# Performance work log

Measured on AMD Instinct MI355X. Metric: run time of the kernel, lower is better.

## Reference

```python
import jax, jax.numpy as jnp
import numpy as np

N_NODES = 100000
N_EDGES = 1000000
NEG_SLOPE = 0.2


def gat_conv(x, src, dst, W, al, ar, b, res, activation):
    """DGL-style GATConv. res is None (no residual), 'id' (identity residual), or a [in,H*D] matrix."""
    H, D = al.shape
    n = x.shape[0]
    feat = (x @ W).reshape(n, H, D)                      # [N,H,D]
    el = jnp.einsum('nhd,hd->nh', feat, al)              # [N,H]
    er = jnp.einsum('nhd,hd->nh', feat, ar)              # [N,H]
    e = jax.nn.leaky_relu(el[src] + er[dst], NEG_SLOPE)  # [E,H]
    # edge softmax over incoming edges of each dst node
    m = jax.lax.stop_gradient(jax.ops.segment_max(e, dst, num_segments=n))
    ex = jnp.exp(e - m[dst])
    s = jax.ops.segment_sum(ex, dst, num_segments=n)
    alpha = ex / s[dst]                                  # [E,H]
    out = jax.ops.segment_sum(feat[src] * alpha[:, :, None], dst, num_segments=n)  # [N,H,D]
    if res == 'id':
        out = out + x.reshape(n, H, D)
    elif res is not None:
        out = out + (x @ res).reshape(n, H, D)
    out = out + b.reshape(1, H, D)
    if activation is not None:
        out = activation(out)
    return out


def setup_inputs() -> dict:
    key = jax.random.key(0)
    ks = jax.random.split(key, 20)
    F_IN, HID = 128, 32
    H1, H2, H3 = 4, 4, 1
    C = 40
    sc = 0.1
    inp = {
        'x':   jax.random.normal(ks[0], (N_NODES, F_IN), dtype=jnp.float32),
        'src': jax.random.randint(ks[1], (N_EDGES,), 0, N_NODES, dtype=jnp.int32),
        'dst': jax.random.randint(ks[2], (N_EDGES,), 0, N_NODES, dtype=jnp.int32),
        # layer 1: in=128 -> H1*HID=128, no residual, elu
        'W1':  sc * jax.random.normal(ks[3], (F_IN, H1 * HID), dtype=jnp.float32),
        'al1': sc * jax.random.normal(ks[4], (H1, HID), dtype=jnp.float32),
        'ar1': sc * jax.random.normal(ks[5], (H1, HID), dtype=jnp.float32),
        'b1':  jnp.zeros((H1 * HID,), dtype=jnp.float32),
        # layer 2: in=128 -> H2*HID=128, identity residual, elu
        'W2':  sc * jax.random.normal(ks[6], (H1 * HID, H2 * HID), dtype=jnp.float32),
        'al2': sc * jax.random.normal(ks[7], (H2, HID), dtype=jnp.float32),
        'ar2': sc * jax.random.normal(ks[8], (H2, HID), dtype=jnp.float32),
        'b2':  jnp.zeros((H2 * HID,), dtype=jnp.float32),
        # layer 3 (output): in=128 -> H3*HID=32, projected residual, no activation
        'W3':  sc * jax.random.normal(ks[9], (H2 * HID, H3 * HID), dtype=jnp.float32),
        'al3': sc * jax.random.normal(ks[10], (H3, HID), dtype=jnp.float32),
        'ar3': sc * jax.random.normal(ks[11], (H3, HID), dtype=jnp.float32),
        'b3':  jnp.zeros((H3 * HID,), dtype=jnp.float32),
        'res3': sc * jax.random.normal(ks[12], (H2 * HID, H3 * HID), dtype=jnp.float32),
        # final classifier
        'Wfc': sc * jax.random.normal(ks[13], (HID, C), dtype=jnp.float32),
        'bfc': jnp.zeros((C,), dtype=jnp.float32),
    }
    return inp


def reference(x, src, dst, W1, al1, ar1, b1, W2, al2, ar2, b2, W3, al3, ar3, b3, res3, Wfc, bfc):
    n = x.shape[0]
    h = gat_conv(x, src, dst, W1, al1, ar1, b1, None, jax.nn.elu).reshape(n, -1)   # [N, 128]
    h = gat_conv(h, src, dst, W2, al2, ar2, b2, 'id', jax.nn.elu).reshape(n, -1)   # [N, 128]
    h = gat_conv(h, src, dst, W3, al3, ar3, b3, res3, None).mean(axis=1)           # [N, 32]
    return h @ Wfc + bfc                                                           # [N, 40]
```

## Files before the change

kernel.cpp:

```cpp
#include <hip/hip_runtime.h>
#include <cstdint>
#include <cstddef>

#define NN 100000
#define NE 1000000
#define GEMM_BLOCKS 1563
#define TICKET_BLOCKS 3907
#define NB_SCAN 391
#define LOG2E 1.4426950408896340736f

typedef unsigned int uint;
typedef unsigned short ushort;
typedef __attribute__((ext_vector_type(8))) short bfrag;
typedef __attribute__((ext_vector_type(4))) float f32x4;

__device__ __forceinline__ ushort f2bf(float f){
  uint u = __float_as_uint(f);
  u += 0x7fffu + ((u >> 16) & 1u);
  return (ushort)(u >> 16);
}
__device__ __forceinline__ float bflo(uint p){ return __uint_as_float(p << 16); }
__device__ __forceinline__ float bfhi(uint p){ return __uint_as_float(p & 0xffff0000u); }


__device__ __forceinline__ void bfrag_body(const float* __restrict__ B1, const float* __restrict__ B2,
                                           int n1, int n2, int NT, ushort* __restrict__ out, int i){
  if (i >= NT*4*64) return;
  int l = i & 63, ks = (i>>6)&3, nt = i>>8;
  int col = nt*16 + (l&15);
  int k0  = ks*32 + (l>>4)*8;
  const float* B; int stride, c;
  if (col < n1){ B = B1; stride = n1; c = col; }
  else         { B = B2; stride = n2; c = col - n1; }
  ushort v[8];
  #pragma unroll
  for (int j=0;j<8;j++) v[j] = f2bf(B[(size_t)(k0+j)*stride + c]);
  uint4 pk;
  pk.x = (uint)v[0] | ((uint)v[1]<<16);
  pk.y = (uint)v[2] | ((uint)v[3]<<16);
  pk.z = (uint)v[4] | ((uint)v[5]<<16);
  pk.w = (uint)v[6] | ((uint)v[7]<<16);
  *(uint4*)(out + (size_t)i*8) = pk;
}

__global__ __launch_bounds__(256) void k_packs(const float* __restrict__ W1, const float* __restrict__ W2,
                                               const float* __restrict__ W3, const float* __restrict__ res3,
                                               ushort* __restrict__ Bf1, ushort* __restrict__ Bf2,
                                               ushort* __restrict__ Bf3){
  int r = blockIdx.x, t = threadIdx.x;
  if (r < 8)       bfrag_body(W1, nullptr, 128, 0, 8, Bf1, r*256 + t);
  else if (r < 16) bfrag_body(W2, nullptr, 128, 0, 8, Bf2, (r-8)*256 + t);
  else             bfrag_body(W3, res3,    32, 32, 4, Bf3, (r-16)*256 + t);
}


__global__ __launch_bounds__(256, 4)
void k_gemm1_ticket(const float* __restrict__ x, const ushort* __restrict__ Bf1,
                    ushort* __restrict__ featb,
                    const float* __restrict__ al, const float* __restrict__ ar,
                    float* __restrict__ el, float* __restrict__ er,
                    const int* __restrict__ dst, int* __restrict__ cnt4, int* __restrict__ tick){
  int bid = blockIdx.x, t = threadIdx.x;
  if (bid >= GEMM_BLOCKS){
    int e = (bid - GEMM_BLOCKS)*256 + t;
    if (e < NE) tick[e] = atomicAdd(&cnt4[(uint)dst[e]*4u + (e & 3)], 1);
    return;
  }

  int l = t & 63, w = t >> 6;
  int rw = bid*64 + w*16;
  int c = l & 15, g = l >> 4;

  f32x4 acc[8];
  #pragma unroll
  for (int nt=0;nt<8;nt++) acc[nt] = (f32x4){0.f,0.f,0.f,0.f};

  int rowA = rw + c; if (rowA >= NN) rowA = NN-1;
  const float* Ap = x + (size_t)rowA*128 + g*8;
  const bfrag* Bp = (const bfrag*)Bf1;

  #pragma unroll
  for (int ks=0; ks<4; ++ks){
    float4 f0 = *(const float4*)(Ap + ks*32);
    float4 f1 = *(const float4*)(Ap + ks*32 + 4);
    bfrag a;
    a[0]=(short)f2bf(f0.x); a[1]=(short)f2bf(f0.y); a[2]=(short)f2bf(f0.z); a[3]=(short)f2bf(f0.w);
    a[4]=(short)f2bf(f1.x); a[5]=(short)f2bf(f1.y); a[6]=(short)f2bf(f1.z); a[7]=(short)f2bf(f1.w);
    #pragma unroll
    for (int nt=0; nt<8; ++nt){
      bfrag b = Bp[(nt*4+ks)*64 + l];
      acc[nt] = __builtin_amdgcn_mfma_f32_16x16x32_bf16(a, b, acc[nt], 0, 0, 0);
    }
  }

  float alv[4][2], arv[4][2];
  #pragma unroll
  for (int h=0;h<4;h++){
    alv[h][0]=al[h*32+c]*LOG2E;    arv[h][0]=ar[h*32+c]*LOG2E;
    alv[h][1]=al[h*32+16+c]*LOG2E; arv[h][1]=ar[h*32+16+c]*LOG2E;
  }

  #pragma unroll
  for (int reg=0; reg<4; ++reg){
    int row = rw + g*4 + reg;
    bool ok = row < NN;
    #pragma unroll
    for (int h=0;h<4;h++){
      float pl = acc[2*h][reg]*alv[h][0] + acc[2*h+1][reg]*alv[h][1];
      float pr = acc[2*h][reg]*arv[h][0] + acc[2*h+1][reg]*arv[h][1];
      #pragma unroll
      for (int off=1; off<16; off<<=1){ pl += __shfl_xor(pl,off); pr += __shfl_xor(pr,off); }
      if (ok && c==0){ el[(size_t)row*4 + h] = pl; er[(size_t)row*4 + h] = pr; }
    }
    if (ok){
      #pragma unroll
      for (int nt=0; nt<8; ++nt)
        featb[(size_t)row*128 + nt*16 + c] = f2bf(acc[nt][reg]);
    }
  }
}


__global__ __launch_bounds__(256) void k_scan_local(const int* __restrict__ cnt4, int* __restrict__ shoff,
                                                    int* __restrict__ rowptr, int* __restrict__ bsum){
  __shared__ int sm[256];
  int t = threadIdx.x;
  int i = blockIdx.x*256 + t;
  int v = 0;
  if (i < NN){
    int4 cc = ((const int4*)cnt4)[i];
    v = cc.x + cc.y + cc.z + cc.w;
    int4 so;
    so.x = 0; so.y = cc.x; so.z = cc.x + cc.y; so.w = cc.x + cc.y + cc.z;
    ((int4*)shoff)[i] = so;
  }
  sm[t] = v;
  __syncthreads();
  for (int off=1; off<256; off<<=1){
    int u = (t>=off) ? sm[t-off] : 0;
    __syncthreads();
    sm[t] += u;
    __syncthreads();
  }
  if (i < NN) rowptr[i] = sm[t] - v;
  if (t == 255) bsum[blockIdx.x] = sm[255];
}

__global__ __launch_bounds__(512) void k_scan_finish(int* __restrict__ rowptr, const int* __restrict__ bsum){
  __shared__ int sm[512];
  __shared__ int ex[512];
  int t = threadIdx.x;
  int v = (t < NB_SCAN) ? bsum[t] : 0;
  sm[t] = v;
  __syncthreads();
  for (int off=1; off<512; off<<=1){
    int u = (t>=off) ? sm[t-off] : 0;
    __syncthreads();
    sm[t] += u;
    __syncthreads();
  }
  ex[t] = sm[t] - v;
  __syncthreads();
  int i = blockIdx.x*512 + t;
  if (i < NN) rowptr[i] += ex[i>>8];
  else if (i == NN) rowptr[NN] = NE;
}


__global__ __launch_bounds__(256) void k_place_dhist(const int* __restrict__ src, const int* __restrict__ dst,
                                                     const int* __restrict__ rowptr, const int* __restrict__ shoff,
                                                     const int* __restrict__ tick, int* __restrict__ csr,
                                                     int* __restrict__ dbin){
  __shared__ int lh[256];
  int bid = blockIdx.x, t = threadIdx.x;
  if (bid < TICKET_BLOCKS){
    int e = bid*256 + t;
    if (e < NE){
      int d = dst[e];
      csr[rowptr[d] + shoff[(uint)d*4u + (e & 3)] + tick[e]] = src[e];
    }
  } else {
    lh[t] = 0;
    __syncthreads();
    int n = (bid - TICKET_BLOCKS)*256 + t;
    if (n < NN){
      int deg = rowptr[n+1] - rowptr[n];
      atomicAdd(&lh[deg > 255 ? 255 : deg], 1);
    }
    __syncthreads();
    if (lh[t] > 0) atomicAdd(&dbin[t], lh[t]);
  }
}

__global__ __launch_bounds__(256) void k_dscan(int* __restrict__ dbin){
  __shared__ int sm[256];
  int t = threadIdx.x;
  int v = dbin[t];
  sm[t] = v;
  __syncthreads();
  for (int off=1; off<256; off<<=1){
    int u = (t>=off) ? sm[t-off] : 0;
    __syncthreads();
    sm[t] += u;
    __syncthreads();
  }
  dbin[t] = sm[t] - v;
}

__global__ __launch_bounds__(256) void k_dscat(const int* __restrict__ rowptr, int* __restrict__ dbin,
                                               int* __restrict__ perm){
  __shared__ int lh[256];
  __shared__ int lbase[256];
  int t = threadIdx.x;
  lh[t] = 0;
  __syncthreads();
  int n = blockIdx.x*256 + t;
  int bin = -1, lticket = 0;
  if (n < NN){
    int deg = rowptr[n+1] - rowptr[n];
    bin = deg > 255 ? 255 : deg;
    lticket = atomicAdd(&lh[bin], 1);
  }
  __syncthreads();
  if (lh[t] > 0) lbase[t] = atomicAdd(&dbin[t], lh[t]);
  __syncthreads();
  if (n < NN) perm[lbase[bin] + lticket] = n;
}


template<int NT, int NTF, int H>
__device__ __forceinline__ void gemm_body(int bid, const ushort* __restrict__ Ab, const ushort* __restrict__ Bf,
                                          ushort* __restrict__ featb, float* __restrict__ Cres,
                                          const float* __restrict__ al, const float* __restrict__ ar,
                                          float* __restrict__ el, float* __restrict__ er, int M){
  __shared__ ushort Bs[NT*2048];
  int t = threadIdx.x;
  #pragma unroll
  for (int i=0; i<NT; ++i)
    ((uint4*)Bs)[i*256 + t] = ((const uint4*)Bf)[i*256 + t];
  __syncthreads();

  int l = t & 63, w = t >> 6;
  int rw = bid*64 + w*16;
  int c = l & 15, g = l >> 4;

  f32x4 acc[NT];
  #pragma unroll
  for (int nt=0;nt<NT;nt++) acc[nt] = (f32x4){0.f,0.f,0.f,0.f};

  int rowA = rw + c; if (rowA >= M) rowA = M-1;
  const ushort* Ap = Ab + (size_t)rowA*128 + g*8;
  const bfrag* Bp = (const bfrag*)Bs;

  #pragma unroll
  for (int ks=0; ks<4; ++ks){
    bfrag a = *(const bfrag*)(Ap + ks*32);
    #pragma unroll
    for (int nt=0; nt<NT; ++nt){
      bfrag b = Bp[(nt*4+ks)*64 + l];
      acc[nt] = __builtin_amdgcn_mfma_f32_16x16x32_bf16(a, b, acc[nt], 0, 0, 0);
    }
  }

  float alv[H][2], arv[H][2];
  #pragma unroll
  for (int h=0;h<H;h++){
    alv[h][0]=al[h*32+c]*LOG2E;    arv[h][0]=ar[h*32+c]*LOG2E;
    alv[h][1]=al[h*32+16+c]*LOG2E; arv[h][1]=ar[h*32+16+c]*LOG2E;
  }

  #pragma unroll
  for (int reg=0; reg<4; ++reg){
    int row = rw + g*4 + reg;
    bool ok = row < M;
    #pragma unroll
    for (int h=0;h<H;h++){
      float pl = acc[2*h][reg]*alv[h][0] + acc[2*h+1][reg]*alv[h][1];
      float pr = acc[2*h][reg]*arv[h][0] + acc[2*h+1][reg]*arv[h][1];
      #pragma unroll
      for (int off=1; off<16; off<<=1){ pl += __shfl_xor(pl,off); pr += __shfl_xor(pr,off); }
      if (ok && c==0){ el[(size_t)row*H + h] = pl; er[(size_t)row*H + h] = pr; }
    }
    if (ok){
      #pragma unroll
      for (int nt=0; nt<NTF; ++nt)
        featb[(size_t)row*(NTF*16) + nt*16 + c] = f2bf(acc[nt][reg]);
      #pragma unroll
      for (int nt=NTF; nt<NT; ++nt)
        Cres[(size_t)row*((NT-NTF)*16) + (nt-NTF)*16 + c] = acc[nt][reg];
    }
  }
}

template<int NT, int NTF, int H>
__global__ __launch_bounds__(256) void k_gemm_mfma(const ushort* __restrict__ Ab, const ushort* __restrict__ Bf,
                                                   ushort* __restrict__ featb, float* __restrict__ Cres,
                                                   const float* __restrict__ al, const float* __restrict__ ar,
                                                   float* __restrict__ el, float* __restrict__ er, int M){
  gemm_body<NT,NTF,H>(blockIdx.x, Ab, Bf, featb, Cres, al, ar, el, er, M);
}


template<int RK>
__global__ __launch_bounds__(256) void k_agg4(const int* __restrict__ rowptr, const int* __restrict__ csr,
                                              const int* __restrict__ perm,
                                              const ushort* __restrict__ feat,
                                              const float* __restrict__ el, const float* __restrict__ er,
                                              const void* __restrict__ res, const float* __restrict__ bias,
                                              ushort* __restrict__ out, int act){
  int t = threadIdx.x;
  int l15 = t & 15;
  int node = perm[blockIdx.x*16 + (t>>4)];

  int beg = rowptr[node], deg = rowptr[node+1] - beg;
  int hm = l15 >> 2;
  float erh = er[(size_t)node*4 + hm];
  const int* cp = csr + beg;
  uint fo = (uint)l15*8u;

  float ssum = 0.f;
  float a0=0.f,a1=0.f,a2=0.f,a3=0.f,a4=0.f,a5=0.f,a6=0.f,a7=0.f;

  int ei = 0;
  for (; ei+4 <= deg; ei += 4){
    int s0 = cp[ei], s1 = cp[ei+1], s2 = cp[ei+2], s3 = cp[ei+3];
    uint4 p0 = *(const uint4*)(feat + ((uint)s0*128u + fo));
    uint4 p1 = *(const uint4*)(feat + ((uint)s1*128u + fo));
    uint4 p2 = *(const uint4*)(feat + ((uint)s2*128u + fo));
    uint4 p3 = *(const uint4*)(feat + ((uint)s3*128u + fo));
    float v0 = el[(uint)s0*4u + hm] + erh; v0 = fmaxf(v0, 0.2f*v0);
    float v1 = el[(uint)s1*4u + hm] + erh; v1 = fmaxf(v1, 0.2f*v1);
    float v2 = el[(uint)s2*4u + hm] + erh; v2 = fmaxf(v2, 0.2f*v2);
    float v3 = el[(uint)s3*4u + hm] + erh; v3 = fmaxf(v3, 0.2f*v3);
    float w0 = __builtin_amdgcn_exp2f(v0);
    float w1 = __builtin_amdgcn_exp2f(v1);
    float w2 = __builtin_amdgcn_exp2f(v2);
    float w3 = __builtin_amdgcn_exp2f(v3);
    ssum += (w0 + w1) + (w2 + w3);
    a0 += w0*bflo(p0.x) + w1*bflo(p1.x) + w2*bflo(p2.x) + w3*bflo(p3.x);
    a1 += w0*bfhi(p0.x) + w1*bfhi(p1.x) + w2*bfhi(p2.x) + w3*bfhi(p3.x);
    a2 += w0*bflo(p0.y) + w1*bflo(p1.y) + w2*bflo(p2.y) + w3*bflo(p3.y);
    a3 += w0*bfhi(p0.y) + w1*bfhi(p1.y) + w2*bfhi(p2.y) + w3*bfhi(p3.y);
    a4 += w0*bflo(p0.z) + w1*bflo(p1.z) + w2*bflo(p2.z) + w3*bflo(p3.z);
    a5 += w0*bfhi(p0.z) + w1*bfhi(p1.z) + w2*bfhi(p2.z) + w3*bfhi(p3.z);
    a6 += w0*bflo(p0.w) + w1*bflo(p1.w) + w2*bflo(p2.w) + w3*bflo(p3.w);
    a7 += w0*bfhi(p0.w) + w1*bfhi(p1.w) + w2*bfhi(p2.w) + w3*bfhi(p3.w);
  }
  for (; ei < deg; ++ei){
    int s0 = cp[ei];
    uint4 p0 = *(const uint4*)(feat + ((uint)s0*128u + fo));
    float v0 = el[(uint)s0*4u + hm] + erh; v0 = fmaxf(v0, 0.2f*v0);
    float w0 = __builtin_amdgcn_exp2f(v0);
    ssum += w0;
    a0 += w0*bflo(p0.x); a1 += w0*bfhi(p0.x);
    a2 += w0*bflo(p0.y); a3 += w0*bfhi(p0.y);
    a4 += w0*bflo(p0.z); a5 += w0*bfhi(p0.z);
    a6 += w0*bflo(p0.w); a7 += w0*bfhi(p0.w);
  }

  float inv = (deg > 0) ? 1.f/ssum : 0.f;
  float o0=a0*inv, o1=a1*inv, o2=a2*inv, o3=a3*inv;
  float o4=a4*inv, o5=a5*inv, o6=a6*inv, o7=a7*inv;
  if (RK == 1){
    uint4 rv = *(const uint4*)((const ushort*)res + (size_t)node*128 + fo);
    o0 += bflo(rv.x); o1 += bfhi(rv.x); o2 += bflo(rv.y); o3 += bfhi(rv.y);
    o4 += bflo(rv.z); o5 += bfhi(rv.z); o6 += bflo(rv.w); o7 += bfhi(rv.w);
  }
  float4 bv0 = *(const float4*)(bias + l15*8);
  float4 bv1 = *(const float4*)(bias + l15*8 + 4);
  o0 += bv0.x; o1 += bv0.y; o2 += bv0.z; o3 += bv0.w;
  o4 += bv1.x; o5 += bv1.y; o6 += bv1.z; o7 += bv1.w;
  if (act){
    o0 = (o0>0.f)?o0:__expf(o0)-1.f;
    o1 = (o1>0.f)?o1:__expf(o1)-1.f;
    o2 = (o2>0.f)?o2:__expf(o2)-1.f;
    o3 = (o3>0.f)?o3:__expf(o3)-1.f;
    o4 = (o4>0.f)?o4:__expf(o4)-1.f;
    o5 = (o5>0.f)?o5:__expf(o5)-1.f;
    o6 = (o6>0.f)?o6:__expf(o6)-1.f;
    o7 = (o7>0.f)?o7:__expf(o7)-1.f;
  }
  uint4 pk;
  pk.x = (uint)f2bf(o0) | ((uint)f2bf(o1)<<16);
  pk.y = (uint)f2bf(o2) | ((uint)f2bf(o3)<<16);
  pk.z = (uint)f2bf(o4) | ((uint)f2bf(o5)<<16);
  pk.w = (uint)f2bf(o6) | ((uint)f2bf(o7)<<16);
  *(uint4*)(out + (size_t)node*128 + fo) = pk;
}


__global__ __launch_bounds__(256) void k_agg1(const int* __restrict__ rowptr, const int* __restrict__ csr,
                                              const int* __restrict__ perm,
                                              const ushort* __restrict__ feat,
                                              const float* __restrict__ el, const float* __restrict__ er,
                                              const float* __restrict__ res, const float* __restrict__ bias,
                                              float* __restrict__ h3){
  int t = threadIdx.x;
  int l7 = t & 7;
  int node = perm[blockIdx.x*32 + (t>>3)];

  int beg = rowptr[node], deg = rowptr[node+1] - beg;
  float er0 = er[node];
  const int* cp = csr + beg;
  uint fo = (uint)l7*4u;

  float ssum = 0.f, a0=0.f, a1=0.f, a2=0.f, a3=0.f;
  int ei = 0;
  for (; ei+2 <= deg; ei += 2){
    int s0 = cp[ei], s1 = cp[ei+1];
    uint2 p0 = *(const uint2*)(feat + ((uint)s0*32u + fo));
    uint2 p1 = *(const uint2*)(feat + ((uint)s1*32u + fo));
    float v0 = el[s0] + er0; v0 = fmaxf(v0, 0.2f*v0);
    float v1 = el[s1] + er0; v1 = fmaxf(v1, 0.2f*v1);
    float w0 = __builtin_amdgcn_exp2f(v0);
    float w1 = __builtin_amdgcn_exp2f(v1);
    ssum += w0 + w1;
    a0 += w0*bflo(p0.x) + w1*bflo(p1.x);
    a1 += w0*bfhi(p0.x) + w1*bfhi(p1.x);
    a2 += w0*bflo(p0.y) + w1*bflo(p1.y);
    a3 += w0*bfhi(p0.y) + w1*bfhi(p1.y);
  }
  if (ei < deg){
    int s0 = cp[ei];
    uint2 p0 = *(const uint2*)(feat + ((uint)s0*32u + fo));
    float v0 = el[s0] + er0; v0 = fmaxf(v0, 0.2f*v0);
    float w0 = __builtin_amdgcn_exp2f(v0);
    ssum += w0;
    a0 += w0*bflo(p0.x); a1 += w0*bfhi(p0.x);
    a2 += w0*bflo(p0.y); a3 += w0*bfhi(p0.y);
  }

  float inv = (deg > 0) ? 1.f/ssum : 0.f;
  float4 rv = *(const float4*)(res + (size_t)node*32 + fo);
  float4 bv = *(const float4*)(bias + fo);
  float4 ov;
  ov.x = a0*inv + rv.x + bv.x;
  ov.y = a1*inv + rv.y + bv.y;
  ov.z = a2*inv + rv.z + bv.z;
  ov.w = a3*inv + rv.w + bv.w;
  *(float4*)(h3 + (size_t)node*32 + fo) = ov;
}


__global__ __launch_bounds__(256) void k_fc(const float* __restrict__ h, const float* __restrict__ W,
                                            const float* __restrict__ b, float* __restrict__ out){
  __shared__ float Ws[32*40];
  __shared__ float Hs[64][33];
  __shared__ float bs[40];
  int t = threadIdx.x;
  for (int i=t; i<1280; i+=256) Ws[i] = W[i];
  if (t < 40) bs[t] = b[t];
  int n0 = blockIdx.x*64;
  for (int idx=t; idx<512; idx+=256){
    int r = idx>>3, c4 = idx&7;
    float4 v;
    if (n0 + r < NN) v = *(const float4*)(h + (size_t)(n0+r)*32 + c4*4);
    else v = make_float4(0.f,0.f,0.f,0.f);
    Hs[r][c4*4+0]=v.x; Hs[r][c4*4+1]=v.y; Hs[r][c4*4+2]=v.z; Hs[r][c4*4+3]=v.w;
  }
  __syncthreads();
  int n = t>>2, cg = t&3;
  float acc[10];
  #pragma unroll
  for (int j=0;j<10;j++) acc[j] = 0.f;
  #pragma unroll
  for (int k=0;k<32;k++){
    float hv = Hs[n][k];
    #pragma unroll
    for (int j=0;j<10;j++) acc[j] += hv * Ws[k*40 + cg + 4*j];
  }
  int row = n0 + n;
  if (row < NN){
    #pragma unroll
    for (int j=0;j<10;j++) out[(size_t)row*40 + cg + 4*j] = acc[j] + bs[cg+4*j];
  }
}


extern "C" void kernel_launch(void* const* d_in, const int* in_sizes, int n_in,
                              void* d_out, int out_size, void* d_ws, size_t ws_size,
                              hipStream_t stream){
  const float* x    = (const float*)d_in[0];
  const int*   src  = (const int*)  d_in[1];
  const int*   dst  = (const int*)  d_in[2];
  const float* W1   = (const float*)d_in[3];
  const float* al1  = (const float*)d_in[4];
  const float* ar1  = (const float*)d_in[5];
  const float* b1   = (const float*)d_in[6];
  const float* W2   = (const float*)d_in[7];
  const float* al2  = (const float*)d_in[8];
  const float* ar2  = (const float*)d_in[9];
  const float* b2   = (const float*)d_in[10];
  const float* W3   = (const float*)d_in[11];
  const float* al3  = (const float*)d_in[12];
  const float* ar3  = (const float*)d_in[13];
  const float* b3   = (const float*)d_in[14];
  const float* res3 = (const float*)d_in[15];
  const float* Wfc  = (const float*)d_in[16];
  const float* bfc  = (const float*)d_in[17];
  float* out = (float*)d_out;

  char* ws = (char*)d_ws;
  size_t o = 0;
  auto alloc = [&](size_t bytes)->char*{
    char* p = ws + o;
    o += (bytes + 255) & ~(size_t)255;
    return p;
  };
  int*    rowptr = (int*)   alloc((size_t)(NN+1)*4);
  int*    cnt4   = (int*)   alloc((size_t)NN*4*4);
  int*    shoff  = (int*)   alloc((size_t)NN*4*4);
  int*    bsum   = (int*)   alloc(512*4);
  int*    dbin   = (int*)   alloc(256*4);
  int*    perm   = (int*)   alloc((size_t)NN*4);
  int*    tick   = (int*)   alloc((size_t)NE*4);
  int*    csr    = (int*)   alloc((size_t)NE*4);
  float*  el     = (float*) alloc((size_t)NN*4*4);
  float*  er     = (float*) alloc((size_t)NN*4*4);
  ushort* featb  = (ushort*)alloc((size_t)NN*128*2);
  ushort* h1b    = (ushort*)alloc((size_t)NN*128*2);
  ushort* h2b    = (ushort*)alloc((size_t)NN*128*2);
  float*  res3p  = (float*) alloc((size_t)NN*32*4);
  float*  h3     = (float*) alloc((size_t)NN*32*4);
  ushort* Bf1    = (ushort*)alloc((size_t)8*4*64*8*2);
  ushort* Bf2    = (ushort*)alloc((size_t)8*4*64*8*2);
  ushort* Bf3    = (ushort*)alloc((size_t)4*4*64*8*2);
  (void)ws_size; (void)n_in; (void)in_sizes; (void)out_size;

  hipMemsetAsync(cnt4, 0, (size_t)NN*4*4, stream);
  hipMemsetAsync(dbin, 0, 256*4, stream);

  k_packs<<<20, 256, 0, stream>>>(W1, W2, W3, res3, Bf1, Bf2, Bf3);

  k_gemm1_ticket<<<GEMM_BLOCKS+TICKET_BLOCKS, 256, 0, stream>>>(x, Bf1, featb, al1, ar1, el, er,
                                                                dst, cnt4, tick);

  k_scan_local<<<NB_SCAN, 256, 0, stream>>>(cnt4, shoff, rowptr, bsum);
  k_scan_finish<<<(NN+1+511)/512, 512, 0, stream>>>(rowptr, bsum);

  k_place_dhist<<<TICKET_BLOCKS+NB_SCAN, 256, 0, stream>>>(src, dst, rowptr, shoff, tick, csr, dbin);
  k_dscan<<<1, 256, 0, stream>>>(dbin);
  k_dscat<<<NB_SCAN, 256, 0, stream>>>(rowptr, dbin, perm);

  k_agg4<0><<<NN/16, 256, 0, stream>>>(rowptr, csr, perm, featb, el, er, nullptr, b1, h1b, 1);

  k_gemm_mfma<8,8,4><<<GEMM_BLOCKS, 256, 0, stream>>>(h1b, Bf2, featb, nullptr, al2, ar2, el, er, NN);
  k_agg4<1><<<NN/16, 256, 0, stream>>>(rowptr, csr, perm, featb, el, er, h1b, b2, h2b, 1);

  k_gemm_mfma<4,2,1><<<GEMM_BLOCKS, 256, 0, stream>>>(h2b, Bf3, featb, res3p, al3, ar3, el, er, NN);
  k_agg1<<<NN/32, 256, 0, stream>>>(rowptr, csr, perm, featb, el, er, res3p, b3, h3);
  k_fc<<<GEMM_BLOCKS, 256, 0, stream>>>(h3, Wfc, bfc, out);
}
```

Baseline: 295.7 us.

## Vectorize edge ticketing and CSR placement, regroup degree-sort kernels, widen GEMM blocks

The edge ticket and CSR placement passes now handle four edges per thread using int4 loads and stores of dst, src and tick. The slot index still equals e&3, so results are unchanged. The degree histogram now runs alone, and CSR placement is merged with the degree scatter, so placement overlaps perm construction instead of the histogram. The layer-2/3 GEMMs use 512-thread blocks of 128 rows, halving per-block B-fragment staging into LDS. This may cost some occupancy.

```diff
diff --git a/kernel.cpp b/kernel.cpp
--- a/kernel.cpp
+++ b/kernel.cpp
@@ -5,7 +5,8 @@
 #define NN 100000
 #define NE 1000000
 #define GEMM_BLOCKS 1563
-#define TICKET_BLOCKS 3907
+#define GEMM2_BLOCKS 782
+#define TICKET4_BLOCKS 977
 #define NB_SCAN 391
 #define LOG2E 1.4426950408896340736f
 
@@ -62,8 +63,16 @@
                     const int* __restrict__ dst, int* __restrict__ cnt4, int* __restrict__ tick){
   int bid = blockIdx.x, t = threadIdx.x;
   if (bid >= GEMM_BLOCKS){
-    int e = (bid - GEMM_BLOCKS)*256 + t;
-    if (e < NE) tick[e] = atomicAdd(&cnt4[(uint)dst[e]*4u + (e & 3)], 1);
+    int idx = (bid - GEMM_BLOCKS)*256 + t;
+    if (idx < NE/4){
+      int e0 = idx*4;
+      int4 d4 = *(const int4*)(dst + e0);
+      int t0 = atomicAdd(&cnt4[(uint)d4.x*4u + 0u], 1);
+      int t1 = atomicAdd(&cnt4[(uint)d4.y*4u + 1u], 1);
+      int t2 = atomicAdd(&cnt4[(uint)d4.z*4u + 2u], 1);
+      int t3 = atomicAdd(&cnt4[(uint)d4.w*4u + 3u], 1);
+      *(int4*)(tick + e0) = make_int4(t0,t1,t2,t3);
+    }
     return;
   }
 
@@ -167,81 +176,86 @@
 }
 
 
-__global__ __launch_bounds__(256) void k_place_dhist(const int* __restrict__ src, const int* __restrict__ dst,
+__global__ __launch_bounds__(256) void k_dhist(const int* __restrict__ rowptr, int* __restrict__ dbin){
+  __shared__ int lh[256];
+  int t = threadIdx.x;
+  lh[t] = 0;
+  __syncthreads();
+  int n = blockIdx.x*256 + t;
+  if (n < NN){
+    int deg = rowptr[n+1] - rowptr[n];
+    atomicAdd(&lh[deg > 255 ? 255 : deg], 1);
+  }
+  __syncthreads();
+  if (lh[t] > 0) atomicAdd(&dbin[t], lh[t]);
+}
+
+__global__ __launch_bounds__(256) void k_dscan(int* __restrict__ dbin){
+  __shared__ int sm[256];
+  int t = threadIdx.x;
+  int v = dbin[t];
+  sm[t] = v;
+  __syncthreads();
+  for (int off=1; off<256; off<<=1){
+    int u = (t>=off) ? sm[t-off] : 0;
+    __syncthreads();
+    sm[t] += u;
+    __syncthreads();
+  }
+  dbin[t] = sm[t] - v;
+}
+
+__global__ __launch_bounds__(256) void k_place_dscat(const int* __restrict__ src, const int* __restrict__ dst,
                                                      const int* __restrict__ rowptr, const int* __restrict__ shoff,
                                                      const int* __restrict__ tick, int* __restrict__ csr,
-                                                     int* __restrict__ dbin){
-  __shared__ int lh[256];
+                                                     int* __restrict__ dbin, int* __restrict__ perm){
   int bid = blockIdx.x, t = threadIdx.x;
-  if (bid < TICKET_BLOCKS){
-    int e = bid*256 + t;
-    if (e < NE){
-      int d = dst[e];
-      csr[rowptr[d] + shoff[(uint)d*4u + (e & 3)] + tick[e]] = src[e];
+  if (bid < TICKET4_BLOCKS){
+    int idx = bid*256 + t;
+    if (idx < NE/4){
+      int e0 = idx*4;
+      int4 s4 = *(const int4*)(src + e0);
+      int4 d4 = *(const int4*)(dst + e0);
+      int4 t4 = *(const int4*)(tick + e0);
+      csr[rowptr[d4.x] + shoff[(uint)d4.x*4u + 0u] + t4.x] = s4.x;
+      csr[rowptr[d4.y] + shoff[(uint)d4.y*4u + 1u] + t4.y] = s4.y;
+      csr[rowptr[d4.z] + shoff[(uint)d4.z*4u + 2u] + t4.z] = s4.z;
+      csr[rowptr[d4.w] + shoff[(uint)d4.w*4u + 3u] + t4.w] = s4.w;
     }
   } else {
+    __shared__ int lh[256];
+    __shared__ int lbase[256];
     lh[t] = 0;
     __syncthreads();
-    int n = (bid - TICKET_BLOCKS)*256 + t;
+    int n = (bid - TICKET4_BLOCKS)*256 + t;
+    int bin = -1, lticket = 0;
     if (n < NN){
       int deg = rowptr[n+1] - rowptr[n];
-      atomicAdd(&lh[deg > 255 ? 255 : deg], 1);
-    }
-    __syncthreads();
-    if (lh[t] > 0) atomicAdd(&dbin[t], lh[t]);
-  }
-}
-
-__global__ __launch_bounds__(256) void k_dscan(int* __restrict__ dbin){
-  __shared__ int sm[256];
-  int t = threadIdx.x;
-  int v = dbin[t];
-  sm[t] = v;
-  __syncthreads();
-  for (int off=1; off<256; off<<=1){
-    int u = (t>=off) ? sm[t-off] : 0;
-    __syncthreads();
-    sm[t] += u;
-    __syncthreads();
-  }
-  dbin[t] = sm[t] - v;
-}
-
-__global__ __launch_bounds__(256) void k_dscat(const int* __restrict__ rowptr, int* __restrict__ dbin,
-                                               int* __restrict__ perm){
-  __shared__ int lh[256];
-  __shared__ int lbase[256];
-  int t = threadIdx.x;
-  lh[t] = 0;
-  __syncthreads();
-  int n = blockIdx.x*256 + t;
-  int bin = -1, lticket = 0;
-  if (n < NN){
-    int deg = rowptr[n+1] - rowptr[n];
-    bin = deg > 255 ? 255 : deg;
-    lticket = atomicAdd(&lh[bin], 1);
-  }
-  __syncthreads();
-  if (lh[t] > 0) lbase[t] = atomicAdd(&dbin[t], lh[t]);
-  __syncthreads();
-  if (n < NN) perm[lbase[bin] + lticket] = n;
+      bin = deg > 255 ? 255 : deg;
+      lticket = atomicAdd(&lh[bin], 1);
+    }
+    __syncthreads();
+    if (lh[t] > 0) lbase[t] = atomicAdd(&dbin[t], lh[t]);
+    __syncthreads();
+    if (n < NN) perm[lbase[bin] + lticket] = n;
+  }
 }
 
 
 template<int NT, int NTF, int H>
-__device__ __forceinline__ void gemm_body(int bid, const ushort* __restrict__ Ab, const ushort* __restrict__ Bf,
-                                          ushort* __restrict__ featb, float* __restrict__ Cres,
-                                          const float* __restrict__ al, const float* __restrict__ ar,
-                                          float* __restrict__ el, float* __restrict__ er, int M){
+__global__ __launch_bounds__(512) void k_gemm_mfma(const ushort* __restrict__ Ab, const ushort* __restrict__ Bf,
+                                                   ushort* __restrict__ featb, float* __restrict__ Cres,
+                                                   const float* __restrict__ al, const float* __restrict__ ar,
+                                                   float* __restrict__ el, float* __restrict__ er, int M){
   __shared__ ushort Bs[NT*2048];
   int t = threadIdx.x;
   #pragma unroll
-  for (int i=0; i<NT; ++i)
-    ((uint4*)Bs)[i*256 + t] = ((const uint4*)Bf)[i*256 + t];
+  for (int i=0; i<NT/2; ++i)
+    ((uint4*)Bs)[i*512 + t] = ((const uint4*)Bf)[i*512 + t];
   __syncthreads();
 
   int l = t & 63, w = t >> 6;
-  int rw = bid*64 + w*16;
+  int rw = blockIdx.x*128 + w*16;
   int c = l & 15, g = l >> 4;
 
   f32x4 acc[NT];
@@ -290,14 +304,6 @@
         Cres[(size_t)row*((NT-NTF)*16) + (nt-NTF)*16 + c] = acc[nt][reg];
     }
   }
-}
-
-template<int NT, int NTF, int H>
-__global__ __launch_bounds__(256) void k_gemm_mfma(const ushort* __restrict__ Ab, const ushort* __restrict__ Bf,
-                                                   ushort* __restrict__ featb, float* __restrict__ Cres,
-                                                   const float* __restrict__ al, const float* __restrict__ ar,
-                                                   float* __restrict__ el, float* __restrict__ er, int M){
-  gemm_body<NT,NTF,H>(blockIdx.x, Ab, Bf, featb, Cres, al, ar, el, er, M);
 }
 
 
@@ -532,22 +538,23 @@
 
   k_packs<<<20, 256, 0, stream>>>(W1, W2, W3, res3, Bf1, Bf2, Bf3);
 
-  k_gemm1_ticket<<<GEMM_BLOCKS+TICKET_BLOCKS, 256, 0, stream>>>(x, Bf1, featb, al1, ar1, el, er,
-                                                                dst, cnt4, tick);
+  k_gemm1_ticket<<<GEMM_BLOCKS+TICKET4_BLOCKS, 256, 0, stream>>>(x, Bf1, featb, al1, ar1, el, er,
+                                                                 dst, cnt4, tick);
 
   k_scan_local<<<NB_SCAN, 256, 0, stream>>>(cnt4, shoff, rowptr, bsum);
   k_scan_finish<<<(NN+1+511)/512, 512, 0, stream>>>(rowptr, bsum);
 
-  k_place_dhist<<<TICKET_BLOCKS+NB_SCAN, 256, 0, stream>>>(src, dst, rowptr, shoff, tick, csr, dbin);
+  k_dhist<<<NB_SCAN, 256, 0, stream>>>(rowptr, dbin);
   k_dscan<<<1, 256, 0, stream>>>(dbin);
-  k_dscat<<<NB_SCAN, 256, 0, stream>>>(rowptr, dbin, perm);
+  k_place_dscat<<<TICKET4_BLOCKS+NB_SCAN, 256, 0, stream>>>(src, dst, rowptr, shoff, tick, csr,
+                                                            dbin, perm);
 
   k_agg4<0><<<NN/16, 256, 0, stream>>>(rowptr, csr, perm, featb, el, er, nullptr, b1, h1b, 1);
 
-  k_gemm_mfma<8,8,4><<<GEMM_BLOCKS, 256, 0, stream>>>(h1b, Bf2, featb, nullptr, al2, ar2, el, er, NN);
+  k_gemm_mfma<8,8,4><<<GEMM2_BLOCKS, 512, 0, stream>>>(h1b, Bf2, featb, nullptr, al2, ar2, el, er, NN);
   k_agg4<1><<<NN/16, 256, 0, stream>>>(rowptr, csr, perm, featb, el, er, h1b, b2, h2b, 1);
 
-  k_gemm_mfma<4,2,1><<<GEMM_BLOCKS, 256, 0, stream>>>(h2b, Bf3, featb, res3p, al3, ar3, el, er, NN);
+  k_gemm_mfma<4,2,1><<<GEMM2_BLOCKS, 512, 0, stream>>>(h2b, Bf3, featb, res3p, al3, ar3, el, er, NN);
   k_agg1<<<NN/32, 256, 0, stream>>>(rowptr, csr, perm, featb, el, er, res3p, b3, h3);
   k_fc<<<GEMM_BLOCKS, 256, 0, stream>>>(h3, Wfc, bfc, out);
 }
```

Result: no change. 298.0 us (+0.8%).
